# Performance work log

Measured on AMD Instinct MI355X. Metric: run time of the kernel, lower is better.

The kernel has to match this reference:

```python
import math
import jax, jax.numpy as jnp
import numpy as np

C, NH, NL, NP, NLAYERS, FFN = 256, 8, 3, 4, 6, 1024
DH = C // NH
SHAPES = ((64, 64), (32, 32), (16, 16))  # (H,W) for res3, res4, res5
SIZES = [h * w for h, w in SHAPES]
STARTS = np.cumsum([0] + SIZES[:-1]).tolist()
EPS = 1e-5


def _sin_pe(H, W):
    d = C // 4
    y = jnp.arange(H, dtype=jnp.float32)[:, None]
    x = jnp.arange(W, dtype=jnp.float32)[None, :]
    div = jnp.exp(jnp.arange(d, dtype=jnp.float32) * (-math.log(10000.0) / d))[:, None, None]
    pe = jnp.concatenate([
        jnp.broadcast_to(jnp.sin(y * div), (d, H, W)),
        jnp.broadcast_to(jnp.cos(y * div), (d, H, W)),
        jnp.broadcast_to(jnp.sin(x * div), (d, H, W)),
        jnp.broadcast_to(jnp.cos(x * div), (d, H, W)),
    ], axis=0)  # (C,H,W)
    return pe.reshape(C, H * W).T  # (HW, C)


def _ref_points():
    pts = []
    for H, W in SHAPES:
        y = jnp.linspace(0.5 / H, 1.0 - 0.5 / H, H)
        x = jnp.linspace(0.5 / W, 1.0 - 0.5 / W, W)
        ry, rx = jnp.meshgrid(y, x, indexing='ij')
        pts.append(jnp.stack([rx.ravel(), ry.ravel()], -1))
    return jnp.concatenate(pts, 0)[None, :, None, :]  # (1,N,1,2), same per level


def _layernorm(x, g, b):
    mu = x.mean(-1, keepdims=True)
    v = ((x - mu) ** 2).mean(-1, keepdims=True)
    return (x - mu) * jax.lax.rsqrt(v + EPS) * g + b


def _bilinear(v, loc, H, W):
    # v: (B,HW,NH,DH); loc: (B,N,NH,NP,2) in [0,1]; grid_sample align_corners=False, zero pad
    B, N = loc.shape[0], loc.shape[1]
    x = loc[..., 0] * W - 0.5
    y = loc[..., 1] * H - 0.5
    x0 = jnp.floor(x); y0 = jnp.floor(y)
    wx = x - x0; wy = y - y0
    x0i = x0.astype(jnp.int32); y0i = y0.astype(jnp.int32)
    v_t = jnp.transpose(v, (0, 2, 1, 3))  # (B,NH,HW,DH)

    def corner(xi, yi, w):
        valid = (xi >= 0) & (xi < W) & (yi >= 0) & (yi < H)
        idx = jnp.clip(yi, 0, H - 1) * W + jnp.clip(xi, 0, W - 1)  # (B,N,NH,NP)
        idx = jnp.transpose(idx, (0, 2, 1, 3)).reshape(B, NH, N * NP)
        g = jnp.take_along_axis(v_t, idx[..., None], axis=2)  # (B,NH,N*NP,DH)
        g = g.reshape(B, NH, N, NP, DH).transpose(0, 2, 1, 3, 4)
        return g * (w * valid)[..., None]

    return (corner(x0i, y0i, (1 - wx) * (1 - wy))
            + corner(x0i + 1, y0i, wx * (1 - wy))
            + corner(x0i, y0i + 1, (1 - wx) * wy)
            + corner(x0i + 1, y0i + 1, wx * wy))


def _forward(res2, res3, res4, res5, level_embed, off_W, off_b, aw_W, aw_b, val_W, val_b,
             out_W, out_b, ln1_g, ln1_b, fc1_W, fc1_b, fc2_W, fc2_b, ln2_g, ln2_b,
             lat_W, lat_b, sm_W, sm_b, gn_g, gn_b):
    feats = [res3, res4, res5]
    B = res3.shape[0]
    flat = jnp.concatenate(
        [f.reshape(B, C, -1).transpose(0, 2, 1) + level_embed[i] for i, f in enumerate(feats)], 1)
    pe = jnp.concatenate([_sin_pe(H, W) for H, W in SHAPES], 0)[None]  # (1,N,C)
    ref = _ref_points()  # (1,N,1,2)
    normalizer = jnp.array([[W, H] for H, W in SHAPES], jnp.float32)  # (NL,2) as (W,H)
    N = flat.shape[1]

    x = flat
    for l in range(NLAYERS):
        q = x + pe
        value = (x @ val_W[l].T + val_b[l]).reshape(B, N, NH, DH)
        off = (q @ off_W[l].T + off_b[l]).reshape(B, N, NH, NL, NP, 2)
        aw = jax.nn.softmax((q @ aw_W[l].T + aw_b[l]).reshape(B, N, NH, NL * NP), -1)
        aw = aw.reshape(B, N, NH, NL, NP)
        loc = ref[:, :, None, :, None, :] + off / normalizer[None, None, None, :, None, :]
        attn = jnp.zeros((B, N, NH, DH), x.dtype)
        for li, (H, W) in enumerate(SHAPES):
            v_l = value[:, STARTS[li]:STARTS[li] + SIZES[li]]
            samp = _bilinear(v_l, loc[:, :, :, li], H, W)  # (B,N,NH,NP,DH)
            attn = attn + jnp.einsum('bnhpd,bnhp->bnhd', samp, aw[:, :, :, li])
        attn = attn.reshape(B, N, C) @ out_W[l].T + out_b[l]
        x = _layernorm(x + attn, ln1_g[l], ln1_b[l])
        h = jax.nn.relu(x @ fc1_W[l].T + fc1_b[l]) @ fc2_W[l].T + fc2_b[l]
        x = _layernorm(x + h, ln2_g[l], ln2_b[l])

    outs = []
    for li, (H, W) in enumerate(SHAPES):
        tok = x[:, STARTS[li]:STARTS[li] + SIZES[li]]
        outs.append(tok.transpose(0, 2, 1).reshape(B, C, H, W))
    o3, o4, o5 = outs

    r2_lat = jnp.einsum('bchw,oc->bohw', res2, lat_W) + lat_b[None, :, None, None]
    Hr, Wr = res2.shape[2], res2.shape[3]
    r3_up = jax.image.resize(o3, (B, C, Hr, Wr), method='bilinear')
    s = jax.lax.conv_general_dilated(r2_lat + r3_up, sm_W, (1, 1), ((1, 1), (1, 1)),
                                     dimension_numbers=('NCHW', 'OIHW', 'NCHW'))
    s = s + sm_b[None, :, None, None]
    # GroupNorm(32, C)
    g = s.reshape(B, 32, C // 32, Hr, Wr)
    mu = g.mean((2, 3, 4), keepdims=True)
    var = jnp.var(g, axis=(2, 3, 4), keepdims=True)
    g = (g - mu) * jax.lax.rsqrt(var + EPS)
    s = g.reshape(B, C, Hr, Wr) * gn_g[None, :, None, None] + gn_b[None, :, None, None]
    s = jax.nn.gelu(s, approximate=False)
    return s, o3, o4, o5


def setup_inputs() -> dict:
    key = jax.random.key(0)
    ks = jax.random.split(key, 16)
    def rn(k, shape, s=0.02):
        return jax.random.normal(k, shape, jnp.float32) * s
    B = 2
    L = NLAYERS
    return {
        'res2': jax.random.normal(ks[0], (B, C, 128, 128), jnp.float32),
        'res3': jax.random.normal(ks[1], (B, C, 64, 64), jnp.float32),
        'res4': jax.random.normal(ks[2], (B, C, 32, 32), jnp.float32),
        'res5': jax.random.normal(ks[3], (B, C, 16, 16), jnp.float32),
        'level_embed': rn(ks[4], (NL, C)),
        'off_W': rn(ks[5], (L, NH * NL * NP * 2, C)), 'off_b': jnp.zeros((L, NH * NL * NP * 2)),
        'aw_W': rn(ks[6], (L, NH * NL * NP, C)), 'aw_b': jnp.zeros((L, NH * NL * NP)),
        'val_W': rn(ks[7], (L, C, C)), 'val_b': jnp.zeros((L, C)),
        'out_W': rn(ks[8], (L, C, C)), 'out_b': jnp.zeros((L, C)),
        'ln1_g': jnp.ones((L, C)), 'ln1_b': jnp.zeros((L, C)),
        'fc1_W': rn(ks[9], (L, FFN, C)), 'fc1_b': jnp.zeros((L, FFN)),
        'fc2_W': rn(ks[10], (L, C, FFN)), 'fc2_b': jnp.zeros((L, C)),
        'ln2_g': jnp.ones((L, C)), 'ln2_b': jnp.zeros((L, C)),
        'lat_W': rn(ks[11], (C, C)), 'lat_b': jnp.zeros((C,)),
        'sm_W': rn(ks[12], (C, C, 3, 3)), 'sm_b': jnp.zeros((C,)),
        'gn_g': jnp.ones((C,)), 'gn_b': jnp.zeros((C,)),
    }


def reference(res2, res3, res4, res5, level_embed, off_W, off_b, aw_W, aw_b, val_W, val_b,
              out_W, out_b, ln1_g, ln1_b, fc1_W, fc1_b, fc2_W, fc2_b, ln2_g, ln2_b,
              lat_W, lat_b, sm_W, sm_b, gn_g, gn_b):
    return _forward(res2, res3, res4, res5, level_embed, off_W, off_b, aw_W, aw_b,
                    val_W, val_b, out_W, out_b, ln1_g, ln1_b, fc1_W, fc1_b, fc2_W, fc2_b,
                    ln2_g, ln2_b, lat_W, lat_b, sm_W, sm_b, gn_g, gn_b)
```

## Files before the change

kernel.cpp:

```cpp
#include <hip/hip_runtime.h>

namespace {
constexpr int Bn   = 2;
constexpr int Cc   = 256;
constexpr int Ntok = 5376;
constexpr int Ffn  = 1024;
constexpr int HW2  = 128 * 128;
constexpr float EPSf = 1e-5f;
constexpr int WL   = 729088;
}

typedef __attribute__((ext_vector_type(8))) short bf16x8;
typedef __attribute__((ext_vector_type(4))) float f32x4;

__device__ inline unsigned short f2bf(float x) {
  unsigned u = __float_as_uint(x);
  return (unsigned short)((u + 0x7fffu + ((u >> 16) & 1u)) >> 16);
}
__device__ inline float bf2f(unsigned short b) {
  return __uint_as_float((unsigned)b << 16);
}

__device__ inline void store_chunk_f32(unsigned short* lds, int row, int g,
                                       const float* v8) {
  int sg = g ^ (row & 7);
  unsigned short tmp[8];
#pragma unroll
  for (int j = 0; j < 8; j++) tmp[j] = f2bf(v8[j]);
  *reinterpret_cast<uint4*>(&lds[row * 64 + sg * 8]) =
      *reinterpret_cast<const uint4*>(tmp);
}
__device__ inline void store_chunk_bf(unsigned short* lds, int row, int g,
                                      uint4 v) {
  int sg = g ^ (row & 7);
  *reinterpret_cast<uint4*>(&lds[row * 64 + sg * 8]) = v;
}

__global__ __launch_bounds__(256) void setup_all(
    const float* __restrict__ r3, const float* __restrict__ r4,
    const float* __restrict__ r5, const float* __restrict__ lemb,
    float* __restrict__ x, unsigned short* __restrict__ xb,
    unsigned short* __restrict__ qb, unsigned short* __restrict__ peb,
    const float* __restrict__ valW, const float* __restrict__ offW,
    const float* __restrict__ awW, const float* __restrict__ outW,
    const float* __restrict__ fc1W, const float* __restrict__ fc2W,
    const float* __restrict__ latW, const float* __restrict__ smW,
    unsigned short* __restrict__ wbf, unsigned short* __restrict__ wlat,
    unsigned short* __restrict__ wt) {
  int bx = blockIdx.x;
  int tid = threadIdx.x;
  if (bx < 1024) {
    const int NPC = Ntok * Cc;
    for (int i = bx * 256 + tid; i < Bn * NPC; i += 1024 * 256) {
      int c = i & 255;
      int rest = i >> 8;
      int p = rest % Ntok;
      int b = rest / Ntok;
      int li = (p < 4096) ? 0 : ((p < 5120) ? 1 : 2);
      int start = (li == 0) ? 0 : ((li == 1) ? 4096 : 5120);
      int size = (li == 0) ? 4096 : ((li == 1) ? 1024 : 256);
      const float* f = (li == 0) ? r3 : ((li == 1) ? r4 : r5);
      int sp = p - start;
      int shift = 6 - li;
      int W = 64 >> li;
      int iy = sp >> shift;
      int ix = sp & (W - 1);
      int j = c & 63;
      int sel = c >> 6;
      float div = expf(-(float)j * (9.210340371976184f / 64.f));
      float coord = (sel < 2) ? (float)iy : (float)ix;
      float arg = coord * div;
      unsigned short pe16 = f2bf((sel & 1) ? cosf(arg) : sinf(arg));
      float v = f[((size_t)(b * Cc + c)) * size + sp] + lemb[li * Cc + c];
      x[i] = v;
      xb[i] = f2bf(v);
      qb[i] = f2bf(v + bf2f(pe16));
      peb[i - b * NPC] = pe16;
    }
    return;
  }
  int b2 = bx - 1024;
  if (b2 < 4272) {
    int i4 = b2 * 256 + tid;
    int l = i4 / 182272;
    int e = (i4 - l * 182272) * 4;
    const float* src;
    int off;
    if (e < 65536) { src = valW + (size_t)l * 65536; off = e; }
    else if (e < 139264) {
      int j = e - 65536;
      if (j < 49152) { src = offW + (size_t)l * 49152; off = j; }
      else { src = awW + (size_t)l * 24576; off = j - 49152; }
    } else if (e < 204800) { src = outW + (size_t)l * 65536; off = e - 139264; }
    else if (e < 466944) { src = fc1W + (size_t)l * 262144; off = e - 204800; }
    else { src = fc2W + (size_t)l * 262144; off = e - 466944; }
    float4 v = *reinterpret_cast<const float4*>(&src[off]);
    unsigned short t[4] = {f2bf(v.x), f2bf(v.y), f2bf(v.z), f2bf(v.w)};
    *reinterpret_cast<uint2*>(&wbf[(size_t)l * WL + e]) =
        *reinterpret_cast<const uint2*>(t);
  } else if (b2 < 4336) {
    int e = ((b2 - 4272) * 256 + tid) * 4;
    float4 v = *reinterpret_cast<const float4*>(&latW[e]);
    unsigned short t[4] = {f2bf(v.x), f2bf(v.y), f2bf(v.z), f2bf(v.w)};
    *reinterpret_cast<uint2*>(&wlat[e]) = *reinterpret_cast<const uint2*>(t);
  } else {
    int i = (b2 - 4336) * 256 + tid;
    int o = i / 2304;
    int r = i - o * 2304;
    int tap = r >> 8;
    int c = r & 255;
    wt[i] = f2bf(smW[((size_t)(o * 256 + c)) * 9 + tap]);
  }
}

template <int ACT, int OBF>
__global__ __launch_bounds__(256) void gemm_mfma_b(
    const unsigned short* __restrict__ A, const unsigned short* __restrict__ Wb,
    const float* __restrict__ bias, void* __restrict__ outp,
    int M, int N, int K, int nbx) {
  __shared__ unsigned short As[64 * 64];
  __shared__ unsigned short Ws[128 * 64];
  const int tid = threadIdx.x;
  const int nwg = gridDim.x;
  const int swz = (blockIdx.x & 7) * (nwg >> 3) + (blockIdx.x >> 3);
  const int m0 = (swz / nbx) * 64, n0 = (swz % nbx) * 128;
  const int wid = tid >> 6, lane = tid & 63;
  const int wm = wid >> 1, wn = wid & 1;
  const int lr = lane & 15, lh = lane >> 4;
  const int r8 = tid >> 3, g8 = tid & 7;
  f32x4 acc[2][4];
#pragma unroll
  for (int i = 0; i < 2; i++)
#pragma unroll
    for (int j = 0; j < 4; j++) acc[i][j] = f32x4{0.f, 0.f, 0.f, 0.f};

  uint4 ra[2], rw[4];
  const uint4 z4 = uint4{0, 0, 0, 0};
#pragma unroll
  for (int i = 0; i < 2; i++)
    ra[i] = *reinterpret_cast<const uint4*>(
        &A[(size_t)(m0 + r8 + i * 32) * K + g8 * 8]);
#pragma unroll
  for (int i = 0; i < 4; i++) {
    int n = n0 + r8 + i * 32;
    rw[i] = (n < N) ? *reinterpret_cast<const uint4*>(
                          &Wb[(size_t)n * K + g8 * 8])
                    : z4;
  }

  for (int k0 = 0; k0 < K; k0 += 64) {
    if (k0) __syncthreads();
#pragma unroll
    for (int i = 0; i < 2; i++) store_chunk_bf(As, r8 + i * 32, g8, ra[i]);
#pragma unroll
    for (int i = 0; i < 4; i++) store_chunk_bf(Ws, r8 + i * 32, g8, rw[i]);
    __syncthreads();
    int kn = k0 + 64;
    if (kn < K) {
#pragma unroll
      for (int i = 0; i < 2; i++)
        ra[i] = *reinterpret_cast<const uint4*>(
            &A[(size_t)(m0 + r8 + i * 32) * K + kn + g8 * 8]);
#pragma unroll
      for (int i = 0; i < 4; i++) {
        int n = n0 + r8 + i * 32;
        rw[i] = (n < N) ? *reinterpret_cast<const uint4*>(
                              &Wb[(size_t)n * K + kn + g8 * 8])
                        : z4;
      }
    }
    bf16x8 af[2][2], bfr[4][2];
#pragma unroll
    for (int mi = 0; mi < 2; mi++) {
      int r = wm * 32 + mi * 16 + lr;
#pragma unroll
      for (int s = 0; s < 2; s++) {
        int g = s * 4 + lh;
        af[mi][s] =
            *reinterpret_cast<const bf16x8*>(&As[r * 64 + (g ^ (r & 7)) * 8]);
      }
    }
#pragma unroll
    for (int nj = 0; nj < 4; nj++) {
      int r = wn * 64 + nj * 16 + lr;
#pragma unroll
      for (int s = 0; s < 2; s++) {
        int g = s * 4 + lh;
        bfr[nj][s] =
            *reinterpret_cast<const bf16x8*>(&Ws[r * 64 + (g ^ (r & 7)) * 8]);
      }
    }
#pragma unroll
    for (int mi = 0; mi < 2; mi++)
#pragma unroll
      for (int nj = 0; nj < 4; nj++) {
        acc[mi][nj] = __builtin_amdgcn_mfma_f32_16x16x32_bf16(
            af[mi][0], bfr[nj][0], acc[mi][nj], 0, 0, 0);
        acc[mi][nj] = __builtin_amdgcn_mfma_f32_16x16x32_bf16(
            af[mi][1], bfr[nj][1], acc[mi][nj], 0, 0, 0);
      }
  }
#pragma unroll
  for (int mi = 0; mi < 2; mi++) {
    int row = m0 + wm * 32 + mi * 16 + lh * 4;
#pragma unroll
    for (int nj = 0; nj < 4; nj++) {
      int col = n0 + wn * 64 + nj * 16 + lr;
      if (col >= N) continue;
      float b = bias[col];
#pragma unroll
      for (int r = 0; r < 4; r++) {
        float v = acc[mi][nj][r] + b;
        if (ACT) v = fmaxf(v, 0.f);
        if (OBF)
          ((unsigned short*)outp)[(size_t)(row + r) * N + col] = f2bf(v);
        else
          ((float*)outp)[(size_t)(row + r) * N + col] = v;
      }
    }
  }
}

template <int WRITEQ, int TOKOUT>
__global__ __launch_bounds__(256) void gemm_ln(
    const unsigned short* __restrict__ A, const unsigned short* __restrict__ Wb,
    const float* __restrict__ bias, const float* __restrict__ g,
    const float* __restrict__ bta, float* __restrict__ x,
    unsigned short* __restrict__ xb, const unsigned short* __restrict__ peb,
    unsigned short* __restrict__ qb, int K, float* __restrict__ o3,
    float* __restrict__ o4, float* __restrict__ o5) {
  __shared__ unsigned short As[32 * 64];
  __shared__ unsigned short Ws[256 * 64];
  __shared__ float pred[2][2][16];
  __shared__ float qred[2][2][16];
  const int tid = threadIdx.x;
  const int swz = (blockIdx.x & 7) * 42 + (blockIdx.x >> 3);
  const int m0 = swz * 32;
  const int wid = tid >> 6, lane = tid & 63;
  const int wm = wid >> 1, wn = wid & 1;
  const int lr = lane & 15, lh = lane >> 4;
  const int r8 = tid >> 3, g8 = tid & 7;
  f32x4 acc[8];
#pragma unroll
  for (int i = 0; i < 8; i++) acc[i] = f32x4{0.f, 0.f, 0.f, 0.f};

  uint4 ra, rw[8];
  ra = *reinterpret_cast<const uint4*>(&A[(size_t)(m0 + r8) * K + g8 * 8]);
#pragma unroll
  for (int i = 0; i < 8; i++)
    rw[i] = *reinterpret_cast<const uint4*>(
        &Wb[(size_t)(r8 + i * 32) * K + g8 * 8]);

  for (int k0 = 0; k0 < K; k0 += 64) {
    if (k0) __syncthreads();
    store_chunk_bf(As, r8, g8, ra);
#pragma unroll
    for (int i = 0; i < 8; i++) store_chunk_bf(Ws, r8 + i * 32, g8, rw[i]);
    __syncthreads();
    int kn = k0 + 64;
    if (kn < K) {
      ra = *reinterpret_cast<const uint4*>(
          &A[(size_t)(m0 + r8) * K + kn + g8 * 8]);
#pragma unroll
      for (int i = 0; i < 8; i++)
        rw[i] = *reinterpret_cast<const uint4*>(
            &Wb[(size_t)(r8 + i * 32) * K + kn + g8 * 8]);
    }
    bf16x8 af[2];
    {
      int r = wm * 16 + lr;
#pragma unroll
      for (int s = 0; s < 2; s++) {
        int gg2 = s * 4 + lh;
        af[s] =
            *reinterpret_cast<const bf16x8*>(&As[r * 64 + (gg2 ^ (r & 7)) * 8]);
      }
    }
#pragma unroll
    for (int nt = 0; nt < 8; nt++) {
      int r = wn * 128 + nt * 16 + lr;
      bf16x8 b0 =
          *reinterpret_cast<const bf16x8*>(&Ws[r * 64 + (lh ^ (r & 7)) * 8]);
      bf16x8 b1 = *reinterpret_cast<const bf16x8*>(
          &Ws[r * 64 + ((4 + lh) ^ (r & 7)) * 8]);
      acc[nt] =
          __builtin_amdgcn_mfma_f32_16x16x32_bf16(af[0], b0, acc[nt], 0, 0, 0);
      acc[nt] =
          __builtin_amdgcn_mfma_f32_16x16x32_bf16(af[1], b1, acc[nt], 0, 0, 0);
    }
  }

  const int rowl = wm * 16 + lh * 4;
#pragma unroll
  for (int nt = 0; nt < 8; nt++) {
    int col = wn * 128 + nt * 16 + lr;
    float bs = bias[col];
#pragma unroll
    for (int r = 0; r < 4; r++)
      acc[nt][r] += bs + x[(size_t)(m0 + rowl + r) * 256 + col];
  }
  float sum[4];
#pragma unroll
  for (int r = 0; r < 4; r++) {
    float s = 0.f;
#pragma unroll
    for (int nt = 0; nt < 8; nt++) s += acc[nt][r];
#pragma unroll
    for (int o = 8; o > 0; o >>= 1) s += __shfl_xor(s, o);
    sum[r] = s;
  }
  if (lr == 0) {
#pragma unroll
    for (int r = 0; r < 4; r++) pred[wm][wn][lh * 4 + r] = sum[r];
  }
  __syncthreads();
  float mu[4];
#pragma unroll
  for (int r = 0; r < 4; r++)
    mu[r] = (pred[wm][0][lh * 4 + r] + pred[wm][1][lh * 4 + r]) * (1.f / 256.f);
  float qs[4];
#pragma unroll
  for (int r = 0; r < 4; r++) {
    float q = 0.f;
#pragma unroll
    for (int nt = 0; nt < 8; nt++) {
      float d = acc[nt][r] - mu[r];
      q += d * d;
    }
#pragma unroll
    for (int o = 8; o > 0; o >>= 1) q += __shfl_xor(q, o);
    qs[r] = q;
  }
  if (lr == 0) {
#pragma unroll
    for (int r = 0; r < 4; r++) qred[wm][wn][lh * 4 + r] = qs[r];
  }
  __syncthreads();
  float rstd[4];
#pragma unroll
  for (int r = 0; r < 4; r++)
    rstd[r] = rsqrtf(
        (qred[wm][0][lh * 4 + r] + qred[wm][1][lh * 4 + r]) * (1.f / 256.f) +
        EPSf);
  float oarr[8][4];
#pragma unroll
  for (int nt = 0; nt < 8; nt++) {
    int col = wn * 128 + nt * 16 + lr;
    float gw = g[col], bw = bta[col];
#pragma unroll
    for (int r = 0; r < 4; r++) {
      int row = m0 + rowl + r;
      size_t idx = (size_t)row * 256 + col;
      float o = (acc[nt][r] - mu[r]) * rstd[r] * gw + bw;
      x[idx] = o;
      xb[idx] = f2bf(o);
      if (WRITEQ) {
        size_t pc = idx - (row >= Ntok ? (size_t)Ntok * 256 : 0);
        qb[idx] = f2bf(o + bf2f(peb[pc]));
      }
      if (TOKOUT) oarr[nt][r] = o;
    }
  }
  if constexpr (TOKOUT) {
    __shared__ float tout[32][129];
    int bb = (m0 >= Ntok) ? 1 : 0;
    int n = m0 - bb * Ntok;
    float* outp;
    int osize, ostart;
    if (n < 4096) { outp = o3; osize = 4096; ostart = 0; }
    else if (n < 5120) { outp = o4; osize = 1024; ostart = 4096; }
    else { outp = o5; osize = 256; ostart = 5120; }
    int sp0 = n - ostart;
#pragma unroll
    for (int hh = 0; hh < 2; hh++) {
      __syncthreads();
      if (wn == hh) {
#pragma unroll
        for (int nt = 0; nt < 8; nt++) {
          int cl = nt * 16 + lr;
#pragma unroll
          for (int r = 0; r < 4; r++) tout[rowl + r][cl] = oarr[nt][r];
        }
      }
      __syncthreads();
      int cl = tid & 127, rh = tid >> 7;
      float* dst =
          outp + ((size_t)(bb * 256 + hh * 128 + cl)) * osize + sp0 + rh * 16;
#pragma unroll
      for (int i = 0; i < 16; i += 4) {
        float4 v4 = {tout[rh * 16 + i + 0][cl], tout[rh * 16 + i + 1][cl],
                     tout[rh * 16 + i + 2][cl], tout[rh * 16 + i + 3][cl]};
        *reinterpret_cast<float4*>(&dst[i]) = v4;
      }
    }
  }
}

__global__ __launch_bounds__(256) void gemm_head(
    const unsigned short* __restrict__ xb, const unsigned short* __restrict__ qb,
    const unsigned short* __restrict__ wv, const unsigned short* __restrict__ wo,
    const float* __restrict__ valB, const float* __restrict__ offB,
    const float* __restrict__ awB, unsigned short* __restrict__ valO,
    float* __restrict__ offO, float* __restrict__ awO) {
  __shared__ unsigned short As[32 * 64];
  __shared__ unsigned short Ws[128 * 64];
  const int tid = threadIdx.x;
  const int swz = (blockIdx.x & 7) * 210 + (blockIdx.x >> 3);
  const bool isval = swz < 672;
  const unsigned short* A;
  const unsigned short* W;
  int m0, n0, Nn;
  if (isval) {
    A = xb; W = wv; Nn = 256;
    m0 = (swz >> 1) * 32; n0 = (swz & 1) * 128;
  } else {
    int s = swz - 672;
    A = qb; W = wo; Nn = 288;
    m0 = (s / 3) * 32; n0 = (s % 3) * 128;
  }
  const int wid = tid >> 6, lane = tid & 63;
  const int wm = wid >> 1, wn = wid & 1;
  const int lr = lane & 15, lh = lane >> 4;
  const int r8 = tid >> 3, g8 = tid & 7;
  f32x4 acc[4];
#pragma unroll
  for (int j = 0; j < 4; j++) acc[j] = f32x4{0.f, 0.f, 0.f, 0.f};

  uint4 ra, rw[4];
  const uint4 z4 = uint4{0, 0, 0, 0};
  ra = *reinterpret_cast<const uint4*>(&A[(size_t)(m0 + r8) * 256 + g8 * 8]);
#pragma unroll
  for (int i = 0; i < 4; i++) {
    int n = n0 + r8 + i * 32;
    rw[i] = (n < Nn) ? *reinterpret_cast<const uint4*>(
                           &W[(size_t)n * 256 + g8 * 8])
                     : z4;
  }

  for (int k0 = 0; k0 < 256; k0 += 64) {
    if (k0) __syncthreads();
    store_chunk_bf(As, r8, g8, ra);
#pragma unroll
    for (int i = 0; i < 4; i++) store_chunk_bf(Ws, r8 + i * 32, g8, rw[i]);
    __syncthreads();
    int kn = k0 + 64;
    if (kn < 256) {
      ra = *reinterpret_cast<const uint4*>(
          &A[(size_t)(m0 + r8) * 256 + kn + g8 * 8]);
#pragma unroll
      for (int i = 0; i < 4; i++) {
        int n = n0 + r8 + i * 32;
        rw[i] = (n < Nn) ? *reinterpret_cast<const uint4*>(
                               &W[(size_t)n * 256 + kn + g8 * 8])
                         : z4;
      }
    }
    bf16x8 af[2];
    {
      int r = wm * 16 + lr;
#pragma unroll
      for (int s = 0; s < 2; s++) {
        int gg2 = s * 4 + lh;
        af[s] =
            *reinterpret_cast<const bf16x8*>(&As[r * 64 + (gg2 ^ (r & 7)) * 8]);
      }
    }
#pragma unroll
    for (int nj = 0; nj < 4; nj++) {
      int r = wn * 64 + nj * 16 + lr;
      bf16x8 b0 =
          *reinterpret_cast<const bf16x8*>(&Ws[r * 64 + (lh ^ (r & 7)) * 8]);
      bf16x8 b1 = *reinterpret_cast<const bf16x8*>(
          &Ws[r * 64 + ((4 + lh) ^ (r & 7)) * 8]);
      acc[nj] =
          __builtin_amdgcn_mfma_f32_16x16x32_bf16(af[0], b0, acc[nj], 0, 0, 0);
      acc[nj] =
          __builtin_amdgcn_mfma_f32_16x16x32_bf16(af[1], b1, acc[nj], 0, 0, 0);
    }
  }
  const int row0 = m0 + wm * 16 + lh * 4;
#pragma unroll
  for (int nj = 0; nj < 4; nj++) {
    int col = n0 + wn * 64 + nj * 16 + lr;
    if (isval) {
      float b = valB[col];
#pragma unroll
      for (int r = 0; r < 4; r++)
        valO[(size_t)(row0 + r) * 256 + col] = f2bf(acc[nj][r] + b);
    } else {
      if (col >= 288) continue;
      float b = (col < 192) ? offB[col] : awB[col - 192];
#pragma unroll
      for (int r = 0; r < 4; r++) {
        float v = acc[nj][r] + b;
        if (col < 192)
          offO[(size_t)(row0 + r) * 192 + col] = v;
        else
          awO[(size_t)(row0 + r) * 96 + col - 192] = v;
      }
    }
  }
}

__global__ __launch_bounds__(256) void msda_fused(
    const unsigned short* __restrict__ value, const float* __restrict__ off,
    const float* __restrict__ awl, unsigned short* __restrict__ attn) {
  __shared__ int recI[8][12][4];
  __shared__ float recW[8][12][4];
  __shared__ float els[8][12];
  const int tid = threadIdx.x;
  float e = 0.f;
  int idxr[4];
  float wcr[4];
  int gq = 0, p = 0;
  if (tid < 96) {
    gq = tid / 12;
    p = tid - gq * 12;
    int gid = blockIdx.x * 8 + gq;
    int h = gid & 7;
    int bn = gid >> 3;
    int n = bn % Ntok;
    int b = bn / Ntok;
    int li0 = (n < 4096) ? 0 : ((n < 5120) ? 1 : 2);
    int start0 = (li0 == 0) ? 0 : ((li0 == 1) ? 4096 : 5120);
    int shift = 6 - li0;
    int Wn = 1 << shift;
    int sp = n - start0;
    int iy = sp >> shift;
    int ix = sp & (Wn - 1);
    float refx = (ix + 0.5f) / (float)Wn;
    float refy = (iy + 0.5f) / (float)Wn;
    const float* ap = awl + (size_t)bn * 96 + h * 12;
    float lg[12];
    float mx = -1e30f;
#pragma unroll
    for (int j = 0; j < 12; j++) { lg[j] = ap[j]; mx = fmaxf(mx, lg[j]); }
    e = expf(lg[p] - mx);
    els[gq][p] = e;
    int li = p >> 2;
    int HWl = 64 >> li;
    int st = (li == 0) ? 0 : ((li == 1) ? 4096 : 5120);
    const float* op = off + (size_t)bn * 192 + h * 24;
    float ox = op[p * 2 + 0];
    float oy = op[p * 2 + 1];
    float lx = refx + ox / (float)HWl;
    float ly = refy + oy / (float)HWl;
    float fx = lx * (float)HWl - 0.5f;
    float fy = ly * (float)HWl - 0.5f;
    float x0f = floorf(fx), y0f = floorf(fy);
    float wx = fx - x0f, wy = fy - y0f;
    int ix0 = (int)x0f, iy0 = (int)y0f;
    int base = (b * Ntok + st) * 256 + h * 32;
#pragma unroll
    for (int cr = 0; cr < 4; cr++) {
      int cx = ix0 + (cr & 1);
      int cy = iy0 + (cr >> 1);
      bool valid = (cx >= 0) & (cx < HWl) & (cy >= 0) & (cy < HWl);
      float wc = ((cr & 1) ? wx : 1.f - wx) * ((cr >> 1) ? wy : 1.f - wy);
      int cxc = min(max(cx, 0), HWl - 1);
      int cyc = min(max(cy, 0), HWl - 1);
      idxr[cr] = base + (cyc * HWl + cxc) * 256;
      wcr[cr] = valid ? wc : 0.f;
    }
  }
  __syncthreads();
  if (tid < 96) {
    float ssum = 0.f;
#pragma unroll
    for (int j = 0; j < 12; j++) ssum += els[gq][j];
    float w = e / ssum;
#pragma unroll
    for (int cr = 0; cr < 4; cr++) {
      recI[gq][p][cr] = idxr[cr];
      recW[gq][p][cr] = w * wcr[cr];
    }
  }
  __syncthreads();
  const int grp = tid >> 5, lane = tid & 31;
  const unsigned short* vb = value + lane;
  float acc = 0.f;
#pragma unroll
  for (int pp = 0; pp < 12; pp++) {
    int4 idx = *reinterpret_cast<const int4*>(&recI[grp][pp][0]);
    float4 w = *reinterpret_cast<const float4*>(&recW[grp][pp][0]);
    acc += w.x * bf2f(vb[idx.x]);
    acc += w.y * bf2f(vb[idx.y]);
    acc += w.z * bf2f(vb[idx.z]);
    acc += w.w * bf2f(vb[idx.w]);
  }
  int gid = blockIdx.x * 8 + grp;
  attn[(size_t)gid * 32 + lane] = f2bf(acc);
}

__global__ __launch_bounds__(256) void conv3x3_mfma(
    const unsigned short* __restrict__ T, const unsigned short* __restrict__ Wt,
    const float* __restrict__ bias, unsigned short* __restrict__ out) {
  __shared__ unsigned short As[64 * 64];
  __shared__ unsigned short Ws[128 * 64];
  const int tid = threadIdx.x;
  const int nwg = gridDim.x;
  const int swz = (blockIdx.x & 7) * (nwg >> 3) + (blockIdx.x >> 3);
  const int m0 = (swz >> 1) * 64, n0 = (swz & 1) * 128;
  const int b = m0 >> 14;
  const int p0 = m0 & 16383;
  const int y = p0 >> 7;
  const int x0 = p0 & 127;
  const int wid = tid >> 6, lane = tid & 63;
  const int wm = wid >> 1, wn = wid & 1;
  const int lr = lane & 15, lh = lane >> 4;
  const int r8 = tid >> 3, g8 = tid & 7;
  f32x4 acc[2][4];
#pragma unroll
  for (int i = 0; i < 2; i++)
#pragma unroll
    for (int j = 0; j < 4; j++) acc[i][j] = f32x4{0.f, 0.f, 0.f, 0.f};

  uint4 ra[2], rw[4];
  auto loadA = [&](int kc, uint4* r) {
    int tap = kc >> 2;
    int cb = (kc & 3) * 64;
    int dy = tap / 3 - 1, dx = tap % 3 - 1;
    int yy = y + dy;
#pragma unroll
    for (int i = 0; i < 2; i++) {
      int row = r8 + i * 32;
      int xx = x0 + row + dx;
      uint4 v = uint4{0, 0, 0, 0};
      if (yy >= 0 && yy < 128 && xx >= 0 && xx < 128)
        v = *reinterpret_cast<const uint4*>(
            &T[((size_t)(b * 16384 + yy * 128 + xx)) * 256 + cb + g8 * 8]);
      r[i] = v;
    }
  };
  auto loadW = [&](int kc, uint4* r) {
#pragma unroll
    for (int i = 0; i < 4; i++)
      r[i] = *reinterpret_cast<const uint4*>(
          &Wt[(size_t)(n0 + r8 + i * 32) * 2304 + kc * 64 + g8 * 8]);
  };
  loadA(0, ra);
  loadW(0, rw);

  for (int kc = 0; kc < 36; kc++) {
    if (kc) __syncthreads();
#pragma unroll
    for (int i = 0; i < 2; i++) store_chunk_bf(As, r8 + i * 32, g8, ra[i]);
#pragma unroll
    for (int i = 0; i < 4; i++) store_chunk_bf(Ws, r8 + i * 32, g8, rw[i]);
    __syncthreads();
    if (kc + 1 < 36) {
      loadA(kc + 1, ra);
      loadW(kc + 1, rw);
    }
    bf16x8 af[2][2], bfr[4][2];
#pragma unroll
    for (int mi = 0; mi < 2; mi++) {
      int r = wm * 32 + mi * 16 + lr;
#pragma unroll
      for (int s = 0; s < 2; s++) {
        int g = s * 4 + lh;
        af[mi][s] =
            *reinterpret_cast<const bf16x8*>(&As[r * 64 + (g ^ (r & 7)) * 8]);
      }
    }
#pragma unroll
    for (int nj = 0; nj < 4; nj++) {
      int r = wn * 64 + nj * 16 + lr;
#pragma unroll
      for (int s = 0; s < 2; s++) {
        int g = s * 4 + lh;
        bfr[nj][s] =
            *reinterpret_cast<const bf16x8*>(&Ws[r * 64 + (g ^ (r & 7)) * 8]);
      }
    }
#pragma unroll
    for (int mi = 0; mi < 2; mi++)
#pragma unroll
      for (int nj = 0; nj < 4; nj++) {
        acc[mi][nj] = __builtin_amdgcn_mfma_f32_16x16x32_bf16(
            af[mi][0], bfr[nj][0], acc[mi][nj], 0, 0, 0);
        acc[mi][nj] = __builtin_amdgcn_mfma_f32_16x16x32_bf16(
            af[mi][1], bfr[nj][1], acc[mi][nj], 0, 0, 0);
      }
  }
#pragma unroll
  for (int mi = 0; mi < 2; mi++) {
    int row = m0 + wm * 32 + mi * 16 + lh * 4;
#pragma unroll
    for (int nj = 0; nj < 4; nj++) {
      int col = n0 + wn * 64 + nj * 16 + lr;
      float b = bias[col];
#pragma unroll
      for (int r = 0; r < 4; r++)
        out[(size_t)(row + r) * 256 + col] = f2bf(acc[mi][nj][r] + b);
    }
  }
}

__global__ __launch_bounds__(256) void gemm_tn_mfma(
    const float* __restrict__ A, const unsigned short* __restrict__ Wb,
    const float* __restrict__ bias, const float* __restrict__ x,
    unsigned short* __restrict__ out) {
  __shared__ unsigned short As[64 * 64];
  __shared__ unsigned short Ws[128 * 64];
  const int tid = threadIdx.x;
  const int nwg = gridDim.x;
  const int swz = (blockIdx.x & 7) * (nwg >> 3) + (blockIdx.x >> 3);
  const int m0 = (swz >> 1) * 64, n0 = (swz & 1) * 128;
  const int b = m0 >> 14;
  const int p0 = m0 & 16383;
  const int wid = tid >> 6, lane = tid & 63;
  const int wm = wid >> 1, wn = wid & 1;
  const int lr = lane & 15, lh = lane >> 4;
  const int r8 = tid >> 3, g8 = tid & 7;
  const int arow = tid & 63, agb = tid >> 6;
  f32x4 acc[2][4];
#pragma unroll
  for (int i = 0; i < 2; i++)
#pragma unroll
    for (int j = 0; j < 4; j++) acc[i][j] = f32x4{0.f, 0.f, 0.f, 0.f};

  float va[16];
  uint4 rw[4];
  auto loadA = [&](int k0, float* v) {
#pragma unroll
    for (int i = 0; i < 2; i++) {
      int g = agb + i * 4;
#pragma unroll
      for (int j = 0; j < 8; j++)
        v[i * 8 + j] =
            A[(size_t)(b * 256 + k0 + g * 8 + j) * 16384 + p0 + arow];
    }
  };
  auto loadW = [&](int k0, uint4* r) {
#pragma unroll
    for (int i = 0; i < 4; i++)
      r[i] = *reinterpret_cast<const uint4*>(
          &Wb[(size_t)(n0 + r8 + i * 32) * 256 + k0 + g8 * 8]);
  };
  loadA(0, va);
  loadW(0, rw);

  for (int k0 = 0; k0 < 256; k0 += 64) {
    if (k0) __syncthreads();
#pragma unroll
    for (int i = 0; i < 2; i++)
      store_chunk_f32(As, arow, agb + i * 4, &va[i * 8]);
#pragma unroll
    for (int i = 0; i < 4; i++) store_chunk_bf(Ws, r8 + i * 32, g8, rw[i]);
    __syncthreads();
    int kn = k0 + 64;
    if (kn < 256) {
      loadA(kn, va);
      loadW(kn, rw);
    }
    bf16x8 af[2][2], bfr[4][2];
#pragma unroll
    for (int mi = 0; mi < 2; mi++) {
      int r = wm * 32 + mi * 16 + lr;
#pragma unroll
      for (int s = 0; s < 2; s++) {
        int g = s * 4 + lh;
        af[mi][s] =
            *reinterpret_cast<const bf16x8*>(&As[r * 64 + (g ^ (r & 7)) * 8]);
      }
    }
#pragma unroll
    for (int nj = 0; nj < 4; nj++) {
      int r = wn * 64 + nj * 16 + lr;
#pragma unroll
      for (int s = 0; s < 2; s++) {
        int g = s * 4 + lh;
        bfr[nj][s] =
            *reinterpret_cast<const bf16x8*>(&Ws[r * 64 + (g ^ (r & 7)) * 8]);
      }
    }
#pragma unroll
    for (int mi = 0; mi < 2; mi++)
#pragma unroll
      for (int nj = 0; nj < 4; nj++) {
        acc[mi][nj] = __builtin_amdgcn_mfma_f32_16x16x32_bf16(
            af[mi][0], bfr[nj][0], acc[mi][nj], 0, 0, 0);
        acc[mi][nj] = __builtin_amdgcn_mfma_f32_16x16x32_bf16(
            af[mi][1], bfr[nj][1], acc[mi][nj], 0, 0, 0);
      }
  }
  const float* xbse = x + (size_t)b * Ntok * 256;
#pragma unroll
  for (int mi = 0; mi < 2; mi++) {
    int row0 = m0 + wm * 32 + mi * 16 + lh * 4;
#pragma unroll
    for (int r = 0; r < 4; r++) {
      int p = (row0 + r) & 16383;
      int Y = p >> 7, X = p & 127;
      float yc = Y * 0.5f - 0.25f;
      float y0f = floorf(yc);
      float wy = yc - y0f;
      int y0 = (int)y0f;
      int y0c = min(max(y0, 0), 63), y1c = min(max(y0 + 1, 0), 63);
      float xc = X * 0.5f - 0.25f;
      float x0f = floorf(xc);
      float wx = xc - x0f;
      int xq0 = (int)x0f;
      int x0c = min(max(xq0, 0), 63), x1c = min(max(xq0 + 1, 0), 63);
      const float* r00 = xbse + (size_t)(y0c * 64 + x0c) * 256;
      const float* r01 = xbse + (size_t)(y0c * 64 + x1c) * 256;
      const float* r10 = xbse + (size_t)(y1c * 64 + x0c) * 256;
      const float* r11 = xbse + (size_t)(y1c * 64 + x1c) * 256;
#pragma unroll
      for (int nj = 0; nj < 4; nj++) {
        int col = n0 + wn * 64 + nj * 16 + lr;
        float up = (1.f - wy) * ((1.f - wx) * r00[col] + wx * r01[col]) +
                   wy * ((1.f - wx) * r10[col] + wx * r11[col]);
        out[(size_t)(row0 + r) * 256 + col] =
            f2bf(acc[mi][nj][r] + bias[col] + up);
      }
    }
  }
}

__global__ __launch_bounds__(256) void gn_partial(
    const unsigned short* __restrict__ s, float* __restrict__ part) {
  int blk = blockIdx.x;
  int pr = blk & 15;
  int bg = blk >> 4;
  int g = bg & 31;
  int b = bg >> 5;
  int tid = threadIdx.x;
  float sum = 0.f, sq = 0.f;
  for (int e = pr * 8192 + tid; e < (pr + 1) * 8192; e += 256) {
    int p = e >> 3, cc = e & 7;
    float v = bf2f(s[((size_t)(b * 16384 + p)) * 256 + g * 8 + cc]);
    sum += v;
    sq += v * v;
  }
  __shared__ float rs[256], rq[256];
  rs[tid] = sum;
  rq[tid] = sq;
  __syncthreads();
  for (int st = 128; st > 0; st >>= 1) {
    if (tid < st) { rs[tid] += rs[tid + st]; rq[tid] += rq[tid + st]; }
    __syncthreads();
  }
  if (tid == 0) {
    part[(size_t)blk * 2 + 0] = rs[0];
    part[(size_t)blk * 2 + 1] = rq[0];
  }
}

__global__ void gn_final(const float* __restrict__ part,
                         float* __restrict__ stats) {
  int tid = threadIdx.x;
  if (tid < 64) {
    float s = 0.f, q = 0.f;
    for (int j = 0; j < 16; j++) {
      s += part[(size_t)(tid * 16 + j) * 2 + 0];
      q += part[(size_t)(tid * 16 + j) * 2 + 1];
    }
    float mu = s * (1.f / 131072.f);
    float var = q * (1.f / 131072.f) - mu * mu;
    stats[tid * 2 + 0] = mu;
    stats[tid * 2 + 1] = rsqrtf(var + EPSf);
  }
}

__global__ void gn_apply(const unsigned short* __restrict__ s,
                         const float* __restrict__ stats,
                         const float* __restrict__ gg,
                         const float* __restrict__ gb,
                         float* __restrict__ out) {
  __shared__ float tile[32][33];
  int p0 = blockIdx.x * 32, c0 = blockIdx.y * 32, b = blockIdx.z;
  int tx = threadIdx.x, tyy = threadIdx.y;
  int c = c0 + tx;
  float mu = stats[(b * 32 + (c >> 3)) * 2 + 0];
  float rstd = stats[(b * 32 + (c >> 3)) * 2 + 1];
  float gw = gg[c], bw = gb[c];
  for (int i = tyy; i < 32; i += 8) {
    float v = bf2f(s[((size_t)(b * 16384 + p0 + i)) * 256 + c]);
    v = (v - mu) * rstd * gw + bw;
    v = 0.5f * v * (1.f + erff(v * 0.70710678118654752f));
    tile[i][tx] = v;
  }
  __syncthreads();
  for (int i = tyy; i < 32; i += 8)
    out[((size_t)(b * 256 + c0 + i)) * 16384 + p0 + tx] = tile[tx][i];
}

extern "C" void kernel_launch(void* const* d_in, const int* in_sizes, int n_in,
                              void* d_out, int out_size, void* d_ws,
                              size_t ws_size, hipStream_t stream) {
  (void)in_sizes; (void)n_in; (void)out_size; (void)ws_size;
  const float* res2  = (const float*)d_in[0];
  const float* res3  = (const float*)d_in[1];
  const float* res4  = (const float*)d_in[2];
  const float* res5  = (const float*)d_in[3];
  const float* lemb  = (const float*)d_in[4];
  const float* off_W = (const float*)d_in[5];
  const float* off_b = (const float*)d_in[6];
  const float* aw_W  = (const float*)d_in[7];
  const float* aw_b  = (const float*)d_in[8];
  const float* val_W = (const float*)d_in[9];
  const float* val_b = (const float*)d_in[10];
  const float* out_W = (const float*)d_in[11];
  const float* out_b = (const float*)d_in[12];
  const float* ln1_g = (const float*)d_in[13];
  const float* ln1_b = (const float*)d_in[14];
  const float* fc1_W = (const float*)d_in[15];
  const float* fc1_b = (const float*)d_in[16];
  const float* fc2_W = (const float*)d_in[17];
  const float* fc2_b = (const float*)d_in[18];
  const float* ln2_g = (const float*)d_in[19];
  const float* ln2_b = (const float*)d_in[20];
  const float* lat_W = (const float*)d_in[21];
  const float* lat_b = (const float*)d_in[22];
  const float* sm_W  = (const float*)d_in[23];
  const float* sm_b  = (const float*)d_in[24];
  const float* gn_g  = (const float*)d_in[25];
  const float* gn_b  = (const float*)d_in[26];

  float* ws = (float*)d_ws;
  float*          x      = ws;
  unsigned short* xb     = (unsigned short*)(ws + 2752512);
  unsigned short* peb    = (unsigned short*)(ws + 4128768);
  unsigned short* qb     = (unsigned short*)(ws + 4816896);
  unsigned short* valueb = (unsigned short*)(ws + 6193152);
  float*          offb   = ws + 7569408;
  float*          awl    = ws + 9633792;
  unsigned short* attnb  = (unsigned short*)(ws + 10665984);
  unsigned short* hb     = (unsigned short*)(ws + 14794752);
  unsigned short* tbuf   = hb;
  unsigned short* wtbuf  = (unsigned short*)(ws + 20299776);
  float*          gnpart = ws + 20594688;
  float*          gnstat = ws + 20596736;
  unsigned short* wbf    = (unsigned short*)(ws + 20596864);
  unsigned short* wlat   = wbf + (size_t)6 * WL;
  unsigned short* sbufb  = (unsigned short*)ws;

  float* out_s  = (float*)d_out;
  float* out_o3 = out_s + (size_t)Bn * Cc * HW2;
  float* out_o4 = out_o3 + (size_t)Bn * Cc * 4096;
  float* out_o5 = out_o4 + (size_t)Bn * Cc * 1024;

  const int M = Bn * Ntok;

  setup_all<<<7664, 256, 0, stream>>>(res3, res4, res5, lemb, x, xb, qb, peb,
                                      val_W, off_W, aw_W, out_W, fc1_W, fc2_W,
                                      lat_W, sm_W, wbf, wlat, wtbuf);

  for (int l = 0; l < 6; l++) {
    const unsigned short* wl = wbf + (size_t)l * WL;
    gemm_head<<<1680, 256, 0, stream>>>(
        xb, qb, wl + 0, wl + 65536, val_b + l * 256, off_b + l * 192,
        aw_b + l * 96, valueb, offb, awl);
    msda_fused<<<10752, 256, 0, stream>>>(valueb, offb, awl, attnb);
    gemm_ln<0, 0><<<336, 256, 0, stream>>>(
        attnb, wl + 139264, out_b + l * 256, ln1_g + l * 256, ln1_b + l * 256,
        x, xb, peb, qb, 256, nullptr, nullptr, nullptr);
    gemm_mfma_b<1, 1><<<1344, 256, 0, stream>>>(
        xb, wl + 204800, fc1_b + l * 1024, hb, M, 1024, 256, 8);
    if (l < 5)
      gemm_ln<1, 0><<<336, 256, 0, stream>>>(
          hb, wl + 466944, fc2_b + l * 256, ln2_g + l * 256, ln2_b + l * 256,
          x, xb, peb, qb, 1024, nullptr, nullptr, nullptr);
    else
      gemm_ln<0, 1><<<336, 256, 0, stream>>>(
          hb, wl + 466944, fc2_b + l * 256, ln2_g + l * 256, ln2_b + l * 256,
          x, xb, peb, qb, 1024, out_o3, out_o4, out_o5);
  }

  gemm_tn_mfma<<<1024, 256, 0, stream>>>(res2, wlat, lat_b, x, tbuf);
  conv3x3_mfma<<<1024, 256, 0, stream>>>(tbuf, wtbuf, sm_b, sbufb);
  gn_partial<<<1024, 256, 0, stream>>>(sbufb, gnpart);
  gn_final<<<1, 64, 0, stream>>>(gnpart, gnstat);
  gn_apply<<<dim3(512, 8, 2), dim3(32, 8), 0, stream>>>(sbufb, gnstat, gn_g,
                                                        gn_b, out_s);
}
```

Before: 718.7 us.

## Halve gemm_ln row tile and process 16 queries per MSDA block with paired loads

The GEMM+LayerNorm kernel now works on 16-row tiles instead of 32. Each of the four waves covers 64 output columns, and the row statistics are reduced across all four waves. This doubles the grid to 672 blocks so more CUs stay busy, at the cost of reloading each weight tile twice as often. The MSDA sampling kernel now handles 16 query-heads per block. Each lane gathers two adjacent bf16 channels with a single 32-bit load and writes them packed, which halves the block count and the number of gather instructions.

```diff
diff --git a/kernel.cpp b/kernel.cpp
--- a/kernel.cpp
+++ b/kernel.cpp
@@ -229,23 +229,23 @@
     unsigned short* __restrict__ xb, const unsigned short* __restrict__ peb,
     unsigned short* __restrict__ qb, int K, float* __restrict__ o3,
     float* __restrict__ o4, float* __restrict__ o5) {
-  __shared__ unsigned short As[32 * 64];
+  __shared__ unsigned short As[16 * 64];
   __shared__ unsigned short Ws[256 * 64];
-  __shared__ float pred[2][2][16];
-  __shared__ float qred[2][2][16];
+  __shared__ float pred[4][16];
+  __shared__ float qred[4][16];
   const int tid = threadIdx.x;
-  const int swz = (blockIdx.x & 7) * 42 + (blockIdx.x >> 3);
-  const int m0 = swz * 32;
+  const int swz = (blockIdx.x & 7) * 84 + (blockIdx.x >> 3);
+  const int m0 = swz * 16;
   const int wid = tid >> 6, lane = tid & 63;
-  const int wm = wid >> 1, wn = wid & 1;
   const int lr = lane & 15, lh = lane >> 4;
   const int r8 = tid >> 3, g8 = tid & 7;
-  f32x4 acc[8];
-#pragma unroll
-  for (int i = 0; i < 8; i++) acc[i] = f32x4{0.f, 0.f, 0.f, 0.f};
+  f32x4 acc[4];
+#pragma unroll
+  for (int i = 0; i < 4; i++) acc[i] = f32x4{0.f, 0.f, 0.f, 0.f};
 
   uint4 ra, rw[8];
-  ra = *reinterpret_cast<const uint4*>(&A[(size_t)(m0 + r8) * K + g8 * 8]);
+  if (tid < 128)
+    ra = *reinterpret_cast<const uint4*>(&A[(size_t)(m0 + r8) * K + g8 * 8]);
 #pragma unroll
   for (int i = 0; i < 8; i++)
     rw[i] = *reinterpret_cast<const uint4*>(
@@ -253,14 +253,15 @@
 
   for (int k0 = 0; k0 < K; k0 += 64) {
     if (k0) __syncthreads();
-    store_chunk_bf(As, r8, g8, ra);
+    if (tid < 128) store_chunk_bf(As, r8, g8, ra);
 #pragma unroll
     for (int i = 0; i < 8; i++) store_chunk_bf(Ws, r8 + i * 32, g8, rw[i]);
     __syncthreads();
     int kn = k0 + 64;
     if (kn < K) {
-      ra = *reinterpret_cast<const uint4*>(
-          &A[(size_t)(m0 + r8) * K + kn + g8 * 8]);
+      if (tid < 128)
+        ra = *reinterpret_cast<const uint4*>(
+            &A[(size_t)(m0 + r8) * K + kn + g8 * 8]);
 #pragma unroll
       for (int i = 0; i < 8; i++)
         rw[i] = *reinterpret_cast<const uint4*>(
@@ -268,7 +269,7 @@
     }
     bf16x8 af[2];
     {
-      int r = wm * 16 + lr;
+      int r = lr;
 #pragma unroll
       for (int s = 0; s < 2; s++) {
         int gg2 = s * 4 + lh;
@@ -277,8 +278,8 @@
       }
     }
 #pragma unroll
-    for (int nt = 0; nt < 8; nt++) {
-      int r = wn * 128 + nt * 16 + lr;
+    for (int nt = 0; nt < 4; nt++) {
+      int r = wid * 64 + nt * 16 + lr;
       bf16x8 b0 =
           *reinterpret_cast<const bf16x8*>(&Ws[r * 64 + (lh ^ (r & 7)) * 8]);
       bf16x8 b1 = *reinterpret_cast<const bf16x8*>(
@@ -290,10 +291,10 @@
     }
   }
 
-  const int rowl = wm * 16 + lh * 4;
-#pragma unroll
-  for (int nt = 0; nt < 8; nt++) {
-    int col = wn * 128 + nt * 16 + lr;
+  const int rowl = lh * 4;
+#pragma unroll
+  for (int nt = 0; nt < 4; nt++) {
+    int col = wid * 64 + nt * 16 + lr;
     float bs = bias[col];
 #pragma unroll
     for (int r = 0; r < 4; r++)
@@ -304,26 +305,28 @@
   for (int r = 0; r < 4; r++) {
     float s = 0.f;
 #pragma unroll
-    for (int nt = 0; nt < 8; nt++) s += acc[nt][r];
+    for (int nt = 0; nt < 4; nt++) s += acc[nt][r];
 #pragma unroll
     for (int o = 8; o > 0; o >>= 1) s += __shfl_xor(s, o);
     sum[r] = s;
   }
   if (lr == 0) {
 #pragma unroll
-    for (int r = 0; r < 4; r++) pred[wm][wn][lh * 4 + r] = sum[r];
+    for (int r = 0; r < 4; r++) pred[wid][lh * 4 + r] = sum[r];
   }
   __syncthreads();
   float mu[4];
 #pragma unroll
   for (int r = 0; r < 4; r++)
-    mu[r] = (pred[wm][0][lh * 4 + r] + pred[wm][1][lh * 4 + r]) * (1.f / 256.f);
+    mu[r] = (pred[0][lh * 4 + r] + pred[1][lh * 4 + r] + pred[2][lh * 4 + r] +
+             pred[3][lh * 4 + r]) *
+            (1.f / 256.f);
   float qs[4];
 #pragma unroll
   for (int r = 0; r < 4; r++) {
     float q = 0.f;
 #pragma unroll
-    for (int nt = 0; nt < 8; nt++) {
+    for (int nt = 0; nt < 4; nt++) {
       float d = acc[nt][r] - mu[r];
       q += d * d;
     }
@@ -333,19 +336,20 @@
   }
   if (lr == 0) {
 #pragma unroll
-    for (int r = 0; r < 4; r++) qred[wm][wn][lh * 4 + r] = qs[r];
+    for (int r = 0; r < 4; r++) qred[wid][lh * 4 + r] = qs[r];
   }
   __syncthreads();
   float rstd[4];
 #pragma unroll
   for (int r = 0; r < 4; r++)
-    rstd[r] = rsqrtf(
-        (qred[wm][0][lh * 4 + r] + qred[wm][1][lh * 4 + r]) * (1.f / 256.f) +
-        EPSf);
-  float oarr[8][4];
-#pragma unroll
-  for (int nt = 0; nt < 8; nt++) {
-    int col = wn * 128 + nt * 16 + lr;
+    rstd[r] = rsqrtf((qred[0][lh * 4 + r] + qred[1][lh * 4 + r] +
+                      qred[2][lh * 4 + r] + qred[3][lh * 4 + r]) *
+                         (1.f / 256.f) +
+                     EPSf);
+  float oarr[4][4];
+#pragma unroll
+  for (int nt = 0; nt < 4; nt++) {
+    int col = wid * 64 + nt * 16 + lr;
     float gw = g[col], bw = bta[col];
 #pragma unroll
     for (int r = 0; r < 4; r++) {
@@ -362,7 +366,7 @@
     }
   }
   if constexpr (TOKOUT) {
-    __shared__ float tout[32][129];
+    __shared__ float tout[16][129];
     int bb = (m0 >= Ntok) ? 1 : 0;
     int n = m0 - bb * Ntok;
     float* outp;
@@ -374,10 +378,10 @@
 #pragma unroll
     for (int hh = 0; hh < 2; hh++) {
       __syncthreads();
-      if (wn == hh) {
-#pragma unroll
-        for (int nt = 0; nt < 8; nt++) {
-          int cl = nt * 16 + lr;
+      if ((wid >> 1) == hh) {
+#pragma unroll
+        for (int nt = 0; nt < 4; nt++) {
+          int cl = (wid & 1) * 64 + nt * 16 + lr;
 #pragma unroll
           for (int r = 0; r < 4; r++) tout[rowl + r][cl] = oarr[nt][r];
         }
@@ -385,11 +389,11 @@
       __syncthreads();
       int cl = tid & 127, rh = tid >> 7;
       float* dst =
-          outp + ((size_t)(bb * 256 + hh * 128 + cl)) * osize + sp0 + rh * 16;
-#pragma unroll
-      for (int i = 0; i < 16; i += 4) {
-        float4 v4 = {tout[rh * 16 + i + 0][cl], tout[rh * 16 + i + 1][cl],
-                     tout[rh * 16 + i + 2][cl], tout[rh * 16 + i + 3][cl]};
+          outp + ((size_t)(bb * 256 + hh * 128 + cl)) * osize + sp0 + rh * 8;
+#pragma unroll
+      for (int i = 0; i < 8; i += 4) {
+        float4 v4 = {tout[rh * 8 + i + 0][cl], tout[rh * 8 + i + 1][cl],
+                     tout[rh * 8 + i + 2][cl], tout[rh * 8 + i + 3][cl]};
         *reinterpret_cast<float4*>(&dst[i]) = v4;
       }
     }
@@ -505,18 +509,18 @@
 __global__ __launch_bounds__(256) void msda_fused(
     const unsigned short* __restrict__ value, const float* __restrict__ off,
     const float* __restrict__ awl, unsigned short* __restrict__ attn) {
-  __shared__ int recI[8][12][4];
-  __shared__ float recW[8][12][4];
-  __shared__ float els[8][12];
+  __shared__ int recI[16][12][4];
+  __shared__ float recW[16][12][4];
+  __shared__ float els[16][12];
   const int tid = threadIdx.x;
   float e = 0.f;
   int idxr[4];
   float wcr[4];
   int gq = 0, p = 0;
-  if (tid < 96) {
+  if (tid < 192) {
     gq = tid / 12;
     p = tid - gq * 12;
-    int gid = blockIdx.x * 8 + gq;
+    int gid = blockIdx.x * 16 + gq;
     int h = gid & 7;
     int bn = gid >> 3;
     int n = bn % Ntok;
@@ -564,7 +568,7 @@
     }
   }
   __syncthreads();
-  if (tid < 96) {
+  if (tid < 192) {
     float ssum = 0.f;
 #pragma unroll
     for (int j = 0; j < 12; j++) ssum += els[gq][j];
@@ -576,20 +580,29 @@
     }
   }
   __syncthreads();
-  const int grp = tid >> 5, lane = tid & 31;
-  const unsigned short* vb = value + lane;
-  float acc = 0.f;
+  const int grp = tid >> 4, lane = tid & 15;
+  const unsigned short* vb = value + lane * 2;
+  float acc0 = 0.f, acc1 = 0.f;
 #pragma unroll
   for (int pp = 0; pp < 12; pp++) {
     int4 idx = *reinterpret_cast<const int4*>(&recI[grp][pp][0]);
     float4 w = *reinterpret_cast<const float4*>(&recW[grp][pp][0]);
-    acc += w.x * bf2f(vb[idx.x]);
-    acc += w.y * bf2f(vb[idx.y]);
-    acc += w.z * bf2f(vb[idx.z]);
-    acc += w.w * bf2f(vb[idx.w]);
-  }
-  int gid = blockIdx.x * 8 + grp;
-  attn[(size_t)gid * 32 + lane] = f2bf(acc);
+    unsigned ua = *reinterpret_cast<const unsigned*>(&vb[idx.x]);
+    unsigned ub = *reinterpret_cast<const unsigned*>(&vb[idx.y]);
+    unsigned uc = *reinterpret_cast<const unsigned*>(&vb[idx.z]);
+    unsigned ud = *reinterpret_cast<const unsigned*>(&vb[idx.w]);
+    acc0 += w.x * bf2f((unsigned short)(ua & 0xffff));
+    acc1 += w.x * bf2f((unsigned short)(ua >> 16));
+    acc0 += w.y * bf2f((unsigned short)(ub & 0xffff));
+    acc1 += w.y * bf2f((unsigned short)(ub >> 16));
+    acc0 += w.z * bf2f((unsigned short)(uc & 0xffff));
+    acc1 += w.z * bf2f((unsigned short)(uc >> 16));
+    acc0 += w.w * bf2f((unsigned short)(ud & 0xffff));
+    acc1 += w.w * bf2f((unsigned short)(ud >> 16));
+  }
+  int gid = blockIdx.x * 16 + grp;
+  unsigned outw = (unsigned)f2bf(acc0) | ((unsigned)f2bf(acc1) << 16);
+  *reinterpret_cast<unsigned*>(&attn[(size_t)gid * 32 + lane * 2]) = outw;
 }
 
 __global__ __launch_bounds__(256) void conv3x3_mfma(
@@ -953,18 +966,18 @@
     gemm_head<<<1680, 256, 0, stream>>>(
         xb, qb, wl + 0, wl + 65536, val_b + l * 256, off_b + l * 192,
         aw_b + l * 96, valueb, offb, awl);
-    msda_fused<<<10752, 256, 0, stream>>>(valueb, offb, awl, attnb);
-    gemm_ln<0, 0><<<336, 256, 0, stream>>>(
+    msda_fused<<<5376, 256, 0, stream>>>(valueb, offb, awl, attnb);
+    gemm_ln<0, 0><<<672, 256, 0, stream>>>(
         attnb, wl + 139264, out_b + l * 256, ln1_g + l * 256, ln1_b + l * 256,
         x, xb, peb, qb, 256, nullptr, nullptr, nullptr);
     gemm_mfma_b<1, 1><<<1344, 256, 0, stream>>>(
         xb, wl + 204800, fc1_b + l * 1024, hb, M, 1024, 256, 8);
     if (l < 5)
-      gemm_ln<1, 0><<<336, 256, 0, stream>>>(
+      gemm_ln<1, 0><<<672, 256, 0, stream>>>(
           hb, wl + 466944, fc2_b + l * 256, ln2_g + l * 256, ln2_b + l * 256,
           x, xb, peb, qb, 1024, nullptr, nullptr, nullptr);
     else
-      gemm_ln<0, 1><<<336, 256, 0, stream>>>(
+      gemm_ln<0, 1><<<672, 256, 0, stream>>>(
           hb, wl + 466944, fc2_b + l * 256, ln2_g + l * 256, ln2_b + l * 256,
           x, xb, peb, qb, 1024, out_o3, out_o4, out_o5);
   }
```

New measurement: 671.7 us. 6.5% less time.
